# Kernel optimization log

Hardware: AMD Instinct MI355X
Metric: run time of the kernel (lower is better)

## Reference

```python
import jax, jax.numpy as jnp
import numpy as np

T, B, D, H, A = 256, 512, 128, 128, 8
RUN_COUNT = 1000

def _orth(k, shape, scale):
    w = jax.random.normal(k, shape, jnp.float32)
    q, r = jnp.linalg.qr(w)
    q = q * jnp.sign(jnp.diag(r))[None, :]
    return scale * q

def setup_inputs() -> dict:
    key = jax.random.key(0)
    ks = jax.random.split(key, 12)
    return {
        'hidden': jnp.zeros((B, H), jnp.float32),
        'obs': jax.random.normal(ks[0], (T, B, D), jnp.float32),
        'dones': (jax.random.randint(ks[1], (T, B), 0, 10) == 0),
        'mean_obs': jax.random.normal(ks[2], (D,), jnp.float32) * 0.1,
        'welford_S': jax.random.uniform(ks[3], (D,), jnp.float32) * RUN_COUNT,
        'running_count': RUN_COUNT,
        'W_emb': _orth(ks[4], (D, H), float(np.sqrt(2.0))), 'b_emb': jnp.zeros((H,), jnp.float32),
        'Wi': jax.random.normal(ks[5], (H, 3 * H), jnp.float32) / np.sqrt(H),
        'Wh': jax.random.normal(ks[6], (H, 3 * H), jnp.float32) / np.sqrt(H),
        'bh': jnp.zeros((3 * H,), jnp.float32),
        'W_act': _orth(ks[7], (H, H), 2.0), 'b_act': jnp.zeros((H,), jnp.float32),
        'W_alpha': _orth(ks[8], (H, A), 0.01), 'b_alpha': jnp.zeros((A,), jnp.float32),
        'W_beta': _orth(ks[9], (H, A), 0.01), 'b_beta': jnp.zeros((A,), jnp.float32),
    }

def _welford(M0, S0, count0, xs):
    # sequential Welford update over stacked rows, as in the original lax.scan
    def step(carry, x):
        M, S, c = carry
        c = c + 1.0
        M_new = M + (x - M) / c
        S_new = S + (x - M) * (x - M_new)
        return (M_new, S_new, c), None
    (M, S, c), _ = jax.lax.scan(step, (M0, S0, jnp.asarray(count0, jnp.float32)), xs)
    return M, S, c

def reference(hidden, obs, dones, mean_obs, welford_S, running_count,
              W_emb, b_emb, Wi, Wh, bh, W_act, b_act, W_alpha, b_alpha, W_beta, b_beta):
    # --- running-stat normalization (running_count > 0 branch) ---
    stacked = obs.reshape(-1, obs.shape[-1])  # [T*B, D]
    M, S, c = _welford(mean_obs, welford_S, running_count, stacked)
    var = S / (c - 1.0)
    obs_n = (obs - M) / (jnp.sqrt(var) + 1e-8)
    # --- embedding MLP ---
    emb = jax.nn.relu(obs_n @ W_emb + b_emb)  # [T, B, H]
    # --- GRU scan over time; precompute input-side gate projections (no input bias, flax GRUCell) ---
    xg = emb @ Wi  # [T, B, 3H]
    def gru_step(h, inp):
        x3, reset = inp
        h = jnp.where(reset[:, None], 0.0, h)  # reset carry where done
        hg = h @ Wh + bh
        xr, xz, xn = jnp.split(x3, 3, axis=-1)
        hr, hz, hn = jnp.split(hg, 3, axis=-1)
        r = jax.nn.sigmoid(xr + hr)
        z = jax.nn.sigmoid(xz + hz)
        n = jnp.tanh(xn + r * hn)
        h_new = (1.0 - z) * n + z * h
        return h_new, h_new
    h_last, ys = jax.lax.scan(gru_step, hidden, (xg, dones))  # ys: [T, B, H]
    # --- policy heads ---
    act = jax.nn.relu(ys @ W_act + b_act)
    alpha = jax.nn.softplus(act @ W_alpha + b_alpha) + 1.0
    beta = jax.nn.softplus(act @ W_beta + b_beta) + 1.0
    return h_last, alpha, beta, M, S
```

## Files before the change

### kernel.cpp

```cpp
#include <hip/hip_runtime.h>

#define T_DIM 256
#define B_DIM 512
#define D_DIM 128
#define H_DIM 128
#define A_DIM 8
#define N_ROWS (T_DIM*B_DIM)
#define NT (N_ROWS/16)
#define NWIN 8
#define LOG2E 1.4426950408889634f

typedef __attribute__((ext_vector_type(4))) float f32x4;
typedef __attribute__((ext_vector_type(8))) short bf16x8;
typedef __attribute__((ext_vector_type(4))) short bf16x4;
typedef __attribute__((ext_vector_type(8))) _Float16 f16x8;
typedef __attribute__((ext_vector_type(4))) unsigned u32x4;

#define OFF_PSUM   0ull
#define OFF_PSQ    1048576ull
#define OFF_STATM  2097152ull
#define OFF_STATI  2097664ull
#define OFF_WEMB   2098176ull
#define OFF_WI     2130944ull
#define OFF_WH     2229248ull
#define OFF_WACT   2425856ull
#define OFF_WHEAD  2458624ull
#define OFF_TLO    2462720ull
#define OFF_UH     2463744ull
#define OFF_XG     4194304ull
#define OFF_YS     104857600ull

#define OUT_H      0
#define OUT_ALPHA  65536
#define OUT_BETA   1114112
#define OUT_M      2162688
#define OUT_S      2162816

__device__ inline short f2bf(float x){
  union { float f; unsigned u; } v; v.f = x;
  unsigned r = v.u + 0x7FFFu + ((v.u>>16)&1u);
  return (short)(r>>16);
}
__device__ inline float bf2f(short h){
  union { unsigned u; float f; } v; v.u = ((unsigned)(unsigned short)h)<<16; return v.f;
}

__device__ inline int swz(int row, int col){ return row*136 + (col ^ ((row&7)<<3)); }

__global__ __launch_bounds__(256) void k_partial(const float* __restrict__ obs,
                                                 double* __restrict__ psum,
                                                 double* __restrict__ psq){
  int tid = threadIdx.x; int col = tid & 127; int rh = tid >> 7;
  double s = 0.0, q = 0.0;
  for (int r = blockIdx.x*2 + rh; r < N_ROWS; r += 2048){
    float v = obs[(size_t)r*D_DIM + col];
    s += (double)v; q += (double)v*(double)v;
  }
  __shared__ double ls[256], lq[256];
  ls[tid]=s; lq[tid]=q; __syncthreads();
  if (rh==0){
    psum[(size_t)blockIdx.x*128 + col] = ls[tid] + ls[tid+128];
    psq [(size_t)blockIdx.x*128 + col] = lq[tid] + lq[tid+128];
  }
}

__global__ __launch_bounds__(1024) void k_stats(const double* __restrict__ psum,
                                                const double* __restrict__ psq,
                                                const float* __restrict__ mean_obs,
                                                const float* __restrict__ welfS,
                                                const int* __restrict__ runcnt,
                                                float* __restrict__ outM, float* __restrict__ outS,
                                                float* __restrict__ wsM,  float* __restrict__ wsI){
  int tid = threadIdx.x; int col = tid & 127; int seg = tid >> 7;
  double s=0.0, q=0.0;
  for (int b=seg; b<1024; b+=8){ s += psum[(size_t)b*128+col]; q += psq[(size_t)b*128+col]; }
  __shared__ double ls[1024], lq[1024];
  ls[tid]=s; lq[tid]=q; __syncthreads();
  if (seg==0){
    for (int b=1;b<8;b++){ s += ls[b*128+col]; q += lq[b*128+col]; }
    double c0 = (double)runcnt[0];
    double Nn = (double)N_ROWS;
    double n  = c0 + Nn;
    double M0 = (double)mean_obs[col], S0 = (double)welfS[col];
    double mb = s / Nn;
    double delta = mb - M0;
    double M = M0 + delta * Nn / n;
    double M2b = q - Nn*mb*mb;
    double S = S0 + M2b + delta*delta*c0*Nn/n;
    double var = S / (n - 1.0);
    float inv = (float)(1.0/(sqrt(var)+1e-8));
    outM[col] = (float)M; outS[col] = (float)S;
    wsM[col]  = (float)M; wsI[col]  = inv;
  }
}

__global__ void k_pack_all(const float* __restrict__ W_emb, const float* __restrict__ Wi,
                           const float* __restrict__ Wh,    const float* __restrict__ W_act,
                           const float* __restrict__ W_al,  const float* __restrict__ W_be,
                           short* __restrict__ Bemb, short* __restrict__ BWi,
                           short* __restrict__ BWh,  short* __restrict__ Bact,
                           short* __restrict__ Bhead){
  int gidx = blockIdx.x*256 + threadIdx.x;
  if (gidx >= 133120) return;
  if (gidx >= 131072){
    int idx = gidx - 131072;
    int j = idx & 7, lane = (idx>>3)&63, kb = (idx>>9)&3;
    int k = kb*32 + (lane>>4)*8 + j;
    int n = lane & 15;
    float wv = (n<8) ? W_al[(size_t)k*8 + n] : W_be[(size_t)k*8 + (n-8)];
    Bhead[idx] = f2bf(wv);
    return;
  }
  const float* src; short* dst; int C; int fmt; int idx;
  if (gidx < 16384)      { src=W_emb; dst=Bemb; C=128; fmt=0; idx=gidx; }
  else if (gidx < 65536) { src=Wi;    dst=BWi;  C=384; fmt=0; idx=gidx-16384; }
  else if (gidx < 114688){ src=Wh;    dst=BWh;  C=384; fmt=1; idx=gidx-65536; }
  else                   { src=W_act; dst=Bact; C=128; fmt=0; idx=gidx-114688; }
  int j = idx & 7, lane = (idx>>3)&63, kb = (idx>>9)&3, ct = idx>>11;
  int k = kb*32 + (lane>>4)*8 + j;
  int n = ct*16 + (lane&15);
  float wv = src[(size_t)k*C + n];
  short h;
  if (fmt==0) h = f2bf(wv);
  else {
    wv *= (n < 256) ? LOG2E : (2.f*LOG2E);
    union { _Float16 hf; short s; } u; u.hf = (_Float16)wv; h = u.s;
  }
  dst[idx] = h;
}

__global__ __launch_bounds__(512) void k_sched(const unsigned char* __restrict__ dones,
                                               int* __restrict__ tlo,
                                               unsigned char* __restrict__ usehid){
  int k = blockIdx.x;
  int b = threadIdx.x;
  int t0 = 0, uh = 1;
  if (k > 0){
    for (int t = 32*k; t >= 0; t--){
      if (dones[(size_t)t*B_DIM + b]){ t0 = t; uh = 0; break; }
    }
  }
  usehid[k*B_DIM + b] = (unsigned char)uh;
  __shared__ int red[512];
  red[b] = t0; __syncthreads();
  if (b < 32){
    int m = red[b*16];
    #pragma unroll
    for (int i=1;i<16;i++) m = min(m, red[b*16+i]);
    tlo[k*32 + b] = m;
  }
}

__global__ __launch_bounds__(512) void k_embxg(const float* __restrict__ obs,
                                               const float* __restrict__ wsM,
                                               const float* __restrict__ wsI,
                                               const short* __restrict__ Bemb,
                                               const float* __restrict__ b_emb,
                                               const short* __restrict__ BWi,
                                               const float* __restrict__ bh,
                                               short* __restrict__ xgpk){
  int tid=threadIdx.x, w=tid>>6, lane=tid&63, q=lane>>4, l=lane&15;
  int rt = blockIdx.x;
  int r0 = rt*16;
  __shared__ __align__(16) short obsL[16*136];
  __shared__ __align__(16) short embL[16*136];

  {
    int row = tid>>5, seg = tid&31;
    f32x4 o = *(const f32x4*)(obs + (size_t)(r0+row)*D_DIM + seg*4);
    f32x4 m = *(const f32x4*)(wsM + seg*4);
    f32x4 iv= *(const f32x4*)(wsI + seg*4);
    bf16x4 v;
    v[0]=f2bf((o[0]-m[0])*iv[0]); v[1]=f2bf((o[1]-m[1])*iv[1]);
    v[2]=f2bf((o[2]-m[2])*iv[2]); v[3]=f2bf((o[3]-m[3])*iv[3]);
    *(bf16x4*)&obsL[swz(row, seg*4)] = v;
  }
  __syncthreads();

  bf16x8 A[4];
  #pragma unroll
  for (int kb=0;kb<4;kb++) A[kb] = *(const bf16x8*)&obsL[swz(l, kb*32+q*8)];

  const bf16x8* BE = (const bf16x8*)Bemb;
  f32x4 accE = {0.f,0.f,0.f,0.f};
  #pragma unroll
  for (int kb=0;kb<4;kb++)
    accE = __builtin_amdgcn_mfma_f32_16x16x32_bf16(A[kb], BE[(w*4+kb)*64+lane], accE, 0,0,0);
  {
    float bb = b_emb[w*16 + l];
    #pragma unroll
    for (int r2=0;r2<4;r2++){
      float e = accE[r2] + bb; e = e>0.f ? e : 0.f;
      int b = q*4+r2;
      embL[swz(b, w*16+l)] = f2bf(e);
    }
  }
  __syncthreads();

  bf16x8 A2[4];
  #pragma unroll
  for (int kb=0;kb<4;kb++) A2[kb] = *(const bf16x8*)&embL[swz(l, kb*32+q*8)];

  const bf16x8* BW = (const bf16x8*)BWi;
  bf16x4* xg4 = (bf16x4*)xgpk;
  #pragma unroll
  for (int g=0; g<3; g++){
    int ct = g*8 + w;
    f32x4 acc = {0.f,0.f,0.f,0.f};
    #pragma unroll
    for (int kb=0;kb<4;kb++)
      acc = __builtin_amdgcn_mfma_f32_16x16x32_bf16(A2[kb], BW[(ct*4+kb)*64+lane], acc, 0,0,0);
    int col = ct*16 + l;
    float bb = (g<2) ? bh[col] : 0.f;
    float sc = (g<2) ? LOG2E : (2.f*LOG2E);
    bf16x4 v;
    v[0]=f2bf((acc[0]+bb)*sc); v[1]=f2bf((acc[1]+bb)*sc);
    v[2]=f2bf((acc[2]+bb)*sc); v[3]=f2bf((acc[3]+bb)*sc);
    xg4[((size_t)rt*24 + ct)*64 + lane] = v;
  }
}

#define LDB(g,kb) __builtin_bit_cast(f16x8, pw4[(((g)*8+w)*4+(kb))*64+lane])
__global__
__attribute__((amdgpu_flat_work_group_size(512,512)))
__attribute__((amdgpu_waves_per_eu(2,2)))
void k_gru(const float* __restrict__ hidden,
           const unsigned char* __restrict__ dones,
           const short* __restrict__ xgpk,
           const short* __restrict__ BWh,
           const float* __restrict__ bh,
           const int* __restrict__ tlo,
           const unsigned char* __restrict__ usehid,
           short* __restrict__ yspk,
           float* __restrict__ h_last){
  int tid=threadIdx.x, w=tid>>6, lane=tid&63, q=lane>>4, l=lane&15;
  int kk = blockIdx.x >> 5, bt = blockIdx.x & 31;
  int t_out0 = kk*32;
  int t_end  = t_out0 + 32;
  int t_start = tlo[kk*32 + bt];

  __shared__ __align__(16) _Float16 hF[2][16*136];

  const u32x4* pw4 = (const u32x4*)BWh;
  f16x8 B00 = LDB(0,0), B01 = LDB(0,1), B02 = LDB(0,2), B03 = LDB(0,3);
  f16x8 B10 = LDB(1,0), B11 = LDB(1,1), B12 = LDB(1,2), B13 = LDB(1,3);
  f16x8 B20 = LDB(2,0), B21 = LDB(2,1), B22 = LDB(2,2), B23 = LDB(2,3);

  float bh2c = bh[2*128 + w*16 + l] * (2.f*LOG2E);

  float hv[4];
  #pragma unroll
  for (int r2=0;r2<4;r2++){
    int b = bt*16 + q*4 + r2;
    hv[r2] = usehid[kk*B_DIM + b] ? hidden[(size_t)b*H_DIM + w*16 + l] : 0.f;
  }

  const bf16x4* xgt = (const bf16x4*)xgpk + (((size_t)t_start*32 + bt)*24 + w)*64 + lane;
  const unsigned char* dnp = dones + (size_t)t_start*B_DIM + bt*16 + q*4;
  bf16x4* yst = (bf16x4*)yspk + (((size_t)t_start*32 + bt)*8 + w)*64 + lane;

  bf16x4 xr_c = xgt[0], xz_c = xgt[512], xn_c = xgt[1024];
  unsigned dn_c = *(const unsigned*)dnp;

  for (int t = t_start; t < t_end; t++){
    int buf = t & 1;
    #pragma unroll
    for (int r2=0;r2<4;r2++){
      float hvv = ((dn_c >> (r2*8)) & 255u) ? 0.f : hv[r2];
      hv[r2] = hvv;
      int b = q*4+r2;
      hF[buf][swz(b, w*16+l)] = (_Float16)hvv;
    }
    asm volatile("s_waitcnt lgkmcnt(0)" ::: "memory");
    __builtin_amdgcn_s_barrier();
    asm volatile("" ::: "memory");

    int adv = (t+1 < t_end) ? 1 : 0;
    xgt += (size_t)adv * 49152;
    dnp += adv * B_DIM;
    bf16x4 xr_n = xgt[0], xz_n = xgt[512], xn_n = xgt[1024];
    unsigned dn_n = *(const unsigned*)dnp;

    const _Float16* hb = &hF[buf][0];
    f16x8 A0 = *(const f16x8*)(hb + swz(l,  0 + q*8));
    f16x8 A1 = *(const f16x8*)(hb + swz(l, 32 + q*8));
    f16x8 A2 = *(const f16x8*)(hb + swz(l, 64 + q*8));
    f16x8 A3 = *(const f16x8*)(hb + swz(l, 96 + q*8));

    f32x4 acc0 = {0.f,0.f,0.f,0.f}, acc1 = {0.f,0.f,0.f,0.f}, acc2 = {0.f,0.f,0.f,0.f};
    acc0 = __builtin_amdgcn_mfma_f32_16x16x32_f16(A0, B00, acc0, 0,0,0);
    acc1 = __builtin_amdgcn_mfma_f32_16x16x32_f16(A0, B10, acc1, 0,0,0);
    acc2 = __builtin_amdgcn_mfma_f32_16x16x32_f16(A0, B20, acc2, 0,0,0);
    acc0 = __builtin_amdgcn_mfma_f32_16x16x32_f16(A1, B01, acc0, 0,0,0);
    acc1 = __builtin_amdgcn_mfma_f32_16x16x32_f16(A1, B11, acc1, 0,0,0);
    acc2 = __builtin_amdgcn_mfma_f32_16x16x32_f16(A1, B21, acc2, 0,0,0);
    acc0 = __builtin_amdgcn_mfma_f32_16x16x32_f16(A2, B02, acc0, 0,0,0);
    acc1 = __builtin_amdgcn_mfma_f32_16x16x32_f16(A2, B12, acc1, 0,0,0);
    acc2 = __builtin_amdgcn_mfma_f32_16x16x32_f16(A2, B22, acc2, 0,0,0);
    acc0 = __builtin_amdgcn_mfma_f32_16x16x32_f16(A3, B03, acc0, 0,0,0);
    acc1 = __builtin_amdgcn_mfma_f32_16x16x32_f16(A3, B13, acc1, 0,0,0);
    acc2 = __builtin_amdgcn_mfma_f32_16x16x32_f16(A3, B23, acc2, 0,0,0);

    #pragma unroll
    for (int r2=0;r2<4;r2++){
      float xr = bf2f(xr_c[r2]), xz = bf2f(xz_c[r2]), xn = bf2f(xn_c[r2]);
      float rg = __builtin_amdgcn_rcpf(1.f + __builtin_amdgcn_exp2f(-(xr + acc0[r2])));
      float zg = __builtin_amdgcn_rcpf(1.f + __builtin_amdgcn_exp2f(-(xz + acc1[r2])));
      float e2 = __builtin_amdgcn_exp2f(xn + rg*(acc2[r2] + bh2c));
      float ng = 1.f - 2.f*__builtin_amdgcn_rcpf(e2 + 1.f);
      hv[r2] = ng + zg*(hv[r2] - ng);
    }
    if (t >= t_out0){
      bf16x4 yv;
      yv[0]=f2bf(hv[0]); yv[1]=f2bf(hv[1]); yv[2]=f2bf(hv[2]); yv[3]=f2bf(hv[3]);
      *yst = yv;
    }
    yst += 16384;
    xr_c = xr_n; xz_c = xz_n; xn_c = xn_n; dn_c = dn_n;
  }

  if (kk == NWIN-1){
    #pragma unroll
    for (int r2=0;r2<4;r2++)
      h_last[(size_t)(bt*16+q*4+r2)*H_DIM + w*16 + l] = hv[r2];
  }
}

__global__ __launch_bounds__(256) void k_heads(const short* __restrict__ yspk,
                                               const short* __restrict__ Bact,
                                               const float* __restrict__ b_act,
                                               const short* __restrict__ Bhead,
                                               const float* __restrict__ b_alpha,
                                               const float* __restrict__ b_beta,
                                               float* __restrict__ alpha,
                                               float* __restrict__ beta){
  int tid=threadIdx.x, w=tid>>6, lane=tid&63, q=lane>>4, l=lane&15;
  size_t rt = (size_t)blockIdx.x*4 + w;
  __shared__ __align__(16) short tl[4][16*136];
  const bf16x4* ys4 = (const bf16x4*)yspk;
  #pragma unroll
  for (int ct=0; ct<8; ct++){
    bf16x4 v = ys4[(rt*8+ct)*64+lane];
    #pragma unroll
    for (int r2=0;r2<4;r2++){ int b=q*4+r2; tl[w][swz(b, ct*16+l)] = v[r2]; }
  }
  __syncthreads();
  bf16x8 A[4];
  #pragma unroll
  for (int kb=0;kb<4;kb++) A[kb] = *(const bf16x8*)&tl[w][swz(l, kb*32+q*8)];
  __syncthreads();
  const bf16x8* BA = (const bf16x8*)Bact;
  f32x4 accA[8];
  #pragma unroll
  for (int ct=0;ct<8;ct++){ f32x4 z = {0.f,0.f,0.f,0.f}; accA[ct]=z; }
  #pragma unroll
  for (int ct=0;ct<8;ct++)
    #pragma unroll
    for (int kb=0;kb<4;kb++)
      accA[ct] = __builtin_amdgcn_mfma_f32_16x16x32_bf16(A[kb], BA[(ct*4+kb)*64+lane], accA[ct], 0,0,0);
  #pragma unroll
  for (int ct=0;ct<8;ct++){
    int col = ct*16 + l;
    float bb = b_act[col];
    #pragma unroll
    for (int r2=0;r2<4;r2++){
      float e = accA[ct][r2] + bb; e = e>0.f ? e : 0.f;
      int b = q*4+r2;
      tl[w][swz(b, col)] = f2bf(e);
    }
  }
  __syncthreads();
  bf16x8 A2[4];
  #pragma unroll
  for (int kb=0;kb<4;kb++) A2[kb] = *(const bf16x8*)&tl[w][swz(l, kb*32+q*8)];
  const bf16x8* BHd = (const bf16x8*)Bhead;
  f32x4 acc = {0.f,0.f,0.f,0.f};
  #pragma unroll
  for (int kb=0;kb<4;kb++)
    acc = __builtin_amdgcn_mfma_f32_16x16x32_bf16(A2[kb], BHd[kb*64+lane], acc, 0,0,0);
  float bb = (l<8) ? b_alpha[l] : b_beta[l-8];
  float* dst = (l<8) ? alpha : beta;
  int cc = (l<8) ? l : l-8;
  #pragma unroll
  for (int r2=0;r2<4;r2++){
    float u = acc[r2] + bb;
    float e = __builtin_amdgcn_exp2f(-fabsf(u)*LOG2E);
    float sp = fmaxf(u,0.f) + 0.6931471805599453f*__builtin_amdgcn_logf(1.f + e);
    dst[(rt*16 + q*4 + r2)*8 + cc] = sp + 1.f;
  }
}

extern "C" void kernel_launch(void* const* d_in, const int* in_sizes, int n_in,
                              void* d_out, int out_size, void* d_ws, size_t ws_size,
                              hipStream_t stream){
  const float* hidden   = (const float*)d_in[0];
  const float* obs      = (const float*)d_in[1];
  const unsigned char* dones = (const unsigned char*)d_in[2];
  const float* mean_obs = (const float*)d_in[3];
  const float* welfS    = (const float*)d_in[4];
  const int*   runcnt   = (const int*)d_in[5];
  const float* W_emb = (const float*)d_in[6];
  const float* b_emb = (const float*)d_in[7];
  const float* Wi    = (const float*)d_in[8];
  const float* Wh    = (const float*)d_in[9];
  const float* bh    = (const float*)d_in[10];
  const float* W_act = (const float*)d_in[11];
  const float* b_act = (const float*)d_in[12];
  const float* W_al  = (const float*)d_in[13];
  const float* b_al  = (const float*)d_in[14];
  const float* W_be  = (const float*)d_in[15];
  const float* b_be  = (const float*)d_in[16];
  float* out = (float*)d_out;
  char*  ws  = (char*)d_ws;

  double* psum = (double*)(ws + OFF_PSUM);
  double* psq  = (double*)(ws + OFF_PSQ);
  float*  wsM  = (float*)(ws + OFF_STATM);
  float*  wsI  = (float*)(ws + OFF_STATI);
  short*  Bemb = (short*)(ws + OFF_WEMB);
  short*  BWi  = (short*)(ws + OFF_WI);
  short*  BWh  = (short*)(ws + OFF_WH);
  short*  Bact = (short*)(ws + OFF_WACT);
  short*  Bhead= (short*)(ws + OFF_WHEAD);
  int*    tlo  = (int*)(ws + OFF_TLO);
  unsigned char* uh = (unsigned char*)(ws + OFF_UH);
  short*  xgpk = (short*)(ws + OFF_XG);
  short*  yspk = (short*)(ws + OFF_YS);

  k_partial<<<1024,256,0,stream>>>(obs, psum, psq);
  k_stats<<<1,1024,0,stream>>>(psum, psq, mean_obs, welfS, runcnt,
                               out+OUT_M, out+OUT_S, wsM, wsI);
  k_sched<<<8,512,0,stream>>>(dones, tlo, uh);
  k_pack_all<<<520,256,0,stream>>>(W_emb, Wi, Wh, W_act, W_al, W_be,
                                   Bemb, BWi, BWh, Bact, Bhead);
  k_embxg<<<8192,512,0,stream>>>(obs, wsM, wsI, Bemb, b_emb, BWi, bh, xgpk);
  k_gru<<<256,512,0,stream>>>(hidden, dones, xgpk, BWh, bh, tlo, uh,
                              yspk, out + OUT_H);
  k_heads<<<2048,256,0,stream>>>(yspk, Bact, b_act, Bhead, b_al, b_be,
                                 out + OUT_ALPHA, out + OUT_BETA);
}
```

Baseline: 509.5 us.

## Prefetch GRU inputs two steps ahead, use packed bf16 converts, drop LDS swizzle

The GRU recurrence now prefetches xg gate inputs and done flags two timesteps ahead instead of one, to hide more global-load latency behind the serial step chain. Per-element bf16 rounding is replaced by the hardware v_cvt_pk_bf16_f32 instruction in the xg projection and in the ys stores. The LDS swizzle on the hidden-state buffer is removed in favour of plain padded indexing with precomputed offsets and pointer swapping for double buffering. The deeper prefetch raises register pressure, and dropping the XOR swizzle could cause LDS bank conflicts. Swizzle removal applies to every swz user, not just the GRU.

```diff
diff --git a/kernel.cpp b/kernel.cpp
--- a/kernel.cpp
+++ b/kernel.cpp
@@ -15,6 +15,7 @@
 typedef __attribute__((ext_vector_type(4))) short bf16x4;
 typedef __attribute__((ext_vector_type(8))) _Float16 f16x8;
 typedef __attribute__((ext_vector_type(4))) unsigned u32x4;
+typedef __attribute__((ext_vector_type(2))) unsigned u32x2;
 
 #define OFF_PSUM   0ull
 #define OFF_PSQ    1048576ull
@@ -45,7 +46,13 @@
   union { unsigned u; float f; } v; v.u = ((unsigned)(unsigned short)h)<<16; return v.f;
 }
 
-__device__ inline int swz(int row, int col){ return row*136 + (col ^ ((row&7)<<3)); }
+__device__ inline int swz(int row, int col){ return row*136 + col; }
+
+__device__ inline unsigned cvtpk_bf16(float lo, float hi){
+  unsigned r;
+  asm("v_cvt_pk_bf16_f32 %0, %1, %2" : "=v"(r) : "v"(lo), "v"(hi));
+  return r;
+}
 
 __global__ __launch_bounds__(256) void k_partial(const float* __restrict__ obs,
                                                  double* __restrict__ psum,
@@ -202,7 +209,7 @@
   for (int kb=0;kb<4;kb++) A2[kb] = *(const bf16x8*)&embL[swz(l, kb*32+q*8)];
 
   const bf16x8* BW = (const bf16x8*)BWi;
-  bf16x4* xg4 = (bf16x4*)xgpk;
+  u32x2* xg8 = (u32x2*)xgpk;
   #pragma unroll
   for (int g=0; g<3; g++){
     int ct = g*8 + w;
@@ -213,10 +220,10 @@
     int col = ct*16 + l;
     float bb = (g<2) ? bh[col] : 0.f;
     float sc = (g<2) ? LOG2E : (2.f*LOG2E);
-    bf16x4 v;
-    v[0]=f2bf((acc[0]+bb)*sc); v[1]=f2bf((acc[1]+bb)*sc);
-    v[2]=f2bf((acc[2]+bb)*sc); v[3]=f2bf((acc[3]+bb)*sc);
-    xg4[((size_t)rt*24 + ct)*64 + lane] = v;
+    u32x2 pv;
+    pv[0] = cvtpk_bf16((acc[0]+bb)*sc, (acc[1]+bb)*sc);
+    pv[1] = cvtpk_bf16((acc[2]+bb)*sc, (acc[3]+bb)*sc);
+    xg8[((size_t)rt*24 + ct)*64 + lane] = pv;
   }
 }
 
@@ -261,31 +268,36 @@
 
   bf16x4 xr_c = xgt[0], xz_c = xgt[512], xn_c = xgt[1024];
   unsigned dn_c = *(const unsigned*)dnp;
+  { int a1 = (t_start+1 < t_end) ? 1 : 0; xgt += (size_t)a1*49152; dnp += a1*B_DIM; }
+  bf16x4 xr_n = xgt[0], xz_n = xgt[512], xn_n = xgt[1024];
+  unsigned dn_n = *(const unsigned*)dnp;
+
+  _Float16* hA = &hF[0][0];
+  _Float16* hB = &hF[1][0];
+  const int wo = q*4*136 + w*16 + l;
+  const int ro = l*136 + q*8;
 
   for (int t = t_start; t < t_end; t++){
-    int buf = t & 1;
     #pragma unroll
     for (int r2=0;r2<4;r2++){
       float hvv = ((dn_c >> (r2*8)) & 255u) ? 0.f : hv[r2];
       hv[r2] = hvv;
-      int b = q*4+r2;
-      hF[buf][swz(b, w*16+l)] = (_Float16)hvv;
+      hA[wo + r2*136] = (_Float16)hvv;
     }
     asm volatile("s_waitcnt lgkmcnt(0)" ::: "memory");
     __builtin_amdgcn_s_barrier();
     asm volatile("" ::: "memory");
 
-    int adv = (t+1 < t_end) ? 1 : 0;
-    xgt += (size_t)adv * 49152;
-    dnp += adv * B_DIM;
-    bf16x4 xr_n = xgt[0], xz_n = xgt[512], xn_n = xgt[1024];
-    unsigned dn_n = *(const unsigned*)dnp;
-
-    const _Float16* hb = &hF[buf][0];
-    f16x8 A0 = *(const f16x8*)(hb + swz(l,  0 + q*8));
-    f16x8 A1 = *(const f16x8*)(hb + swz(l, 32 + q*8));
-    f16x8 A2 = *(const f16x8*)(hb + swz(l, 64 + q*8));
-    f16x8 A3 = *(const f16x8*)(hb + swz(l, 96 + q*8));
+    int a2 = (t+2 < t_end) ? 1 : 0;
+    xgt += (size_t)a2 * 49152;
+    dnp += a2 * B_DIM;
+    bf16x4 xr_2 = xgt[0], xz_2 = xgt[512], xn_2 = xgt[1024];
+    unsigned dn_2 = *(const unsigned*)dnp;
+
+    f16x8 A0 = *(const f16x8*)(hA + ro +  0);
+    f16x8 A1 = *(const f16x8*)(hA + ro + 32);
+    f16x8 A2 = *(const f16x8*)(hA + ro + 64);
+    f16x8 A3 = *(const f16x8*)(hA + ro + 96);
 
     f32x4 acc0 = {0.f,0.f,0.f,0.f}, acc1 = {0.f,0.f,0.f,0.f}, acc2 = {0.f,0.f,0.f,0.f};
     acc0 = __builtin_amdgcn_mfma_f32_16x16x32_f16(A0, B00, acc0, 0,0,0);
@@ -311,12 +323,15 @@
       hv[r2] = ng + zg*(hv[r2] - ng);
     }
     if (t >= t_out0){
-      bf16x4 yv;
-      yv[0]=f2bf(hv[0]); yv[1]=f2bf(hv[1]); yv[2]=f2bf(hv[2]); yv[3]=f2bf(hv[3]);
-      *yst = yv;
+      u32x2 pv;
+      pv[0] = cvtpk_bf16(hv[0], hv[1]);
+      pv[1] = cvtpk_bf16(hv[2], hv[3]);
+      *(u32x2*)yst = pv;
     }
     yst += 16384;
     xr_c = xr_n; xz_c = xz_n; xn_c = xn_n; dn_c = dn_n;
+    xr_n = xr_2; xz_n = xz_2; xn_n = xn_2; dn_n = dn_2;
+    _Float16* tmp = hA; hA = hB; hB = tmp;
   }
 
   if (kk == NWIN-1){
```

New measurement: 499.0 us. 1.02x faster.
